# Kernel optimization log

Measured on AMD Instinct MI355X. Metric: run time of the kernel, lower is better.

## Reference

```python
import jax, jax.numpy as jnp
import numpy as np

B, C, C1, C2, H, W = 16, 64, 16, 64, 128, 128

def setup_inputs() -> dict:
    key = jax.random.key(0)
    ks = jax.random.split(key, 8)
    s1 = 1.0 / np.sqrt(C1)
    s2 = 1.0 / np.sqrt(C)
    return {
        "x": jax.random.normal(ks[0], (B, C, H, W), dtype=jnp.float32),
        "e": jax.random.normal(ks[1], (B, C1, H, W), dtype=jnp.float32),
        "W1": jax.random.uniform(ks[2], (C2, C1), jnp.float32, -s1, s1),
        "b1": jax.random.uniform(ks[3], (C2,), jnp.float32, -s1, s1),
        "W2": jax.random.uniform(ks[4], (C2, C), jnp.float32, -s2, s2),
        "b2": jax.random.uniform(ks[5], (C2,), jnp.float32, -s2, s2),
        "W3": jax.random.uniform(ks[6], (C2, C), jnp.float32, -s2, s2),
        "b3": jax.random.uniform(ks[7], (C2,), jnp.float32, -s2, s2),
    }

def _conv1x1(inp, Wm, bv):
    # (B,Cin,H,W) x (Cout,Cin) -> (B,Cout,H,W)
    return jnp.einsum('bchw,oc->bohw', inp, Wm) + bv[None, :, None, None]

def reference(x, e, W1, b1, W2, b2, W3, b3):
    Bn, _, Hn, Wn = x.shape
    Q = _conv1x1(e, W1, b1).reshape(-1, Hn, Wn)   # (B*C2, H, W)
    V = _conv1x1(x, W2, b2).reshape(-1, Hn, Wn)
    K = _conv1x1(x, W3, b3).reshape(-1, Hn, Wn)
    score = jnp.einsum('nhw,ngw->nhg', Q, V)      # (B*C2, H, H), no scaling
    attn = jax.nn.softmax(score, axis=-1)
    ctx = jnp.einsum('nhg,ngw->nhw', attn, K)     # (B*C2, H, W)
    return ctx.reshape(Bn, -1, Hn, Wn)
```

## Files before the change

kernel.cpp:

```cpp
#include <hip/hip_runtime.h>

typedef __bf16 bf16_t;
typedef __bf16 bf16x8 __attribute__((ext_vector_type(8)));
typedef float f32x4 __attribute__((ext_vector_type(4)));
typedef unsigned short u16x4_t __attribute__((ext_vector_type(4)));

#define HW 16384
#define LOG2E 1.44269504088896f

__device__ __forceinline__ bf16_t f2b(float f) {
  unsigned u = __builtin_bit_cast(unsigned, f);
  u += 0x7fff + ((u >> 16) & 1);
  unsigned short s = (unsigned short)(u >> 16);
  return __builtin_bit_cast(bf16_t, s);
}
__device__ __forceinline__ unsigned short b2u(bf16_t b) {
  return __builtin_bit_cast(unsigned short, b);
}
__device__ __forceinline__ int swz8(int row) { return ((row ^ (row >> 3)) & 7) << 4; }
__device__ __forceinline__ int swz4v(int row) { return (row ^ (row >> 2)) & 3; }

__global__ __launch_bounds__(256, 3) void qvk_kernel(
    const float* __restrict__ x, const float* __restrict__ e,
    const float* __restrict__ W1, const float* __restrict__ b1,
    const float* __restrict__ W2, const float* __restrict__ b2,
    const float* __restrict__ W3, const float* __restrict__ b3,
    bf16_t* __restrict__ Qg, bf16_t* __restrict__ Vg, bf16_t* __restrict__ Kg)
{
  __shared__ bf16_t lx[128 * 64];
  __shared__ bf16_t le[128 * 32];
  __shared__ bf16_t w2b[64 * 64];
  __shared__ bf16_t w3b[64 * 64];
  __shared__ bf16_t w1b[64 * 32];

  const int t = threadIdx.x;
  const int lane = t & 63;
  const int wv = t >> 6;
  const int b = blockIdx.x >> 7;
  const int p0 = (blockIdx.x & 127) << 7;
  const int lr = lane & 15;
  const int lg = lane >> 4;
  const int kq = lg << 3;

  const int li = lane & 31;
  const int h2 = lane >> 5;
  const int cbase = wv * 16 + h2 * 8;
  f32x4 xr[8];
#pragma unroll
  for (int j = 0; j < 8; ++j)
    xr[j] = *reinterpret_cast<const f32x4*>(
        x + (size_t)(b * 64 + cbase + j) * HW + p0 + li * 4);

  const int ec = t >> 4;
  const int ep = (t & 15) * 4;
  f32x4 er[2];
#pragma unroll
  for (int j = 0; j < 2; ++j)
    er[j] = *reinterpret_cast<const f32x4*>(
        e + (size_t)(b * 16 + ec) * HW + p0 + ep + j * 64);

  const int wo = t >> 2;
  const int wc = (t & 3) * 16;
  f32x4 w2r[4], w3r[4];
#pragma unroll
  for (int k = 0; k < 4; ++k) {
    w2r[k] = *reinterpret_cast<const f32x4*>(W2 + (size_t)wo * 64 + wc + k * 4);
    w3r[k] = *reinterpret_cast<const f32x4*>(W3 + (size_t)wo * 64 + wc + k * 4);
  }
  const int w1c = (t & 3) * 4;
  f32x4 w1r = *reinterpret_cast<const f32x4*>(W1 + (size_t)wo * 16 + w1c);

  float bv1[4], bv2[4], bv3[4];
#pragma unroll
  for (int nt = 0; nt < 4; ++nt) {
    bv1[nt] = b1[nt * 16 + lr];
    bv2[nt] = b2[nt * 16 + lr];
    bv3[nt] = b3[nt * 16 + lr];
  }

  {
    const int chunk = cbase >> 3;
#pragma unroll
    for (int r = 0; r < 4; ++r) {
      const int row = li * 4 + r;
      bf16x8 v;
#pragma unroll
      for (int j = 0; j < 8; ++j) v[j] = f2b(xr[j][r]);
      *reinterpret_cast<bf16x8*>(reinterpret_cast<char*>(lx)
          + row * 128 + ((chunk << 4) ^ swz8(row))) = v;
    }
  }
#pragma unroll
  for (int j = 0; j < 2; ++j)
#pragma unroll
    for (int r = 0; r < 4; ++r) {
      const int row = ep + j * 64 + r;
      const int byte = row * 64 + ((((ec >> 3) ^ swz4v(row)) << 4)) + (ec & 7) * 2;
      *reinterpret_cast<bf16_t*>(reinterpret_cast<char*>(le) + byte) = f2b(er[j][r]);
    }
  {
    const int row = t >> 1;
    const int chunk = 2 + (t & 1);
    bf16x8 zv;
#pragma unroll
    for (int k = 0; k < 8; ++k) zv[k] = f2b(0.0f);
    *reinterpret_cast<bf16x8*>(reinterpret_cast<char*>(le)
        + row * 64 + ((chunk ^ swz4v(row)) << 4)) = zv;
  }
  {
    const int ch0 = (t & 3) * 2;
    bf16x8 a, c2;
#pragma unroll
    for (int k = 0; k < 8; ++k) {
      a[k]  = f2b(w2r[k >> 2][k & 3]);
      c2[k] = f2b(w2r[2 + (k >> 2)][k & 3]);
    }
    *reinterpret_cast<bf16x8*>(reinterpret_cast<char*>(w2b)
        + wo * 128 + ((ch0 << 4) ^ swz8(wo))) = a;
    *reinterpret_cast<bf16x8*>(reinterpret_cast<char*>(w2b)
        + wo * 128 + (((ch0 + 1) << 4) ^ swz8(wo))) = c2;
#pragma unroll
    for (int k = 0; k < 8; ++k) {
      a[k]  = f2b(w3r[k >> 2][k & 3]);
      c2[k] = f2b(w3r[2 + (k >> 2)][k & 3]);
    }
    *reinterpret_cast<bf16x8*>(reinterpret_cast<char*>(w3b)
        + wo * 128 + ((ch0 << 4) ^ swz8(wo))) = a;
    *reinterpret_cast<bf16x8*>(reinterpret_cast<char*>(w3b)
        + wo * 128 + (((ch0 + 1) << 4) ^ swz8(wo))) = c2;
  }
  {
    typedef __bf16 bf16x4_ __attribute__((ext_vector_type(4)));
    bf16x4_ a;
#pragma unroll
    for (int k = 0; k < 4; ++k) a[k] = f2b(w1r[k]);
    const int byte = wo * 64 + (((w1c >> 3) ^ swz4v(wo)) << 4) + (w1c & 4) * 2;
    *reinterpret_cast<bf16x4_*>(reinterpret_cast<char*>(w1b) + byte) = a;
    if (t < 128) {
      const int row = t >> 1;
      const int chunk = 2 + (t & 1);
      bf16x8 zv;
#pragma unroll
      for (int k = 0; k < 8; ++k) zv[k] = f2b(0.0f);
      *reinterpret_cast<bf16x8*>(reinterpret_cast<char*>(w1b)
          + row * 64 + ((chunk ^ swz4v(row)) << 4)) = zv;
    }
  }
  __syncthreads();

  const int pw0 = wv << 5;

  auto ldx = [&](int row, int ce) -> bf16x8 {
    return *reinterpret_cast<const bf16x8*>(reinterpret_cast<const char*>(lx)
        + row * 128 + (((ce >> 3) << 4) ^ swz8(row)));
  };
  auto ldw = [&](const bf16_t* wb, int row, int ce) -> bf16x8 {
    return *reinterpret_cast<const bf16x8*>(reinterpret_cast<const char*>(wb)
        + row * 128 + (((ce >> 3) << 4) ^ swz8(row)));
  };
  auto ld64 = [&](const bf16_t* buf, int row, int ce) -> bf16x8 {
    return *reinterpret_cast<const bf16x8*>(reinterpret_cast<const char*>(buf)
        + row * 64 + (((ce >> 3) ^ swz4v(row)) << 4));
  };

  f32x4 acc[2][4];

  auto do_xtarget = [&](const bf16_t* wb, const float* bvv, bf16_t* __restrict__ G) {
#pragma unroll
    for (int mt = 0; mt < 2; ++mt)
#pragma unroll
      for (int nt = 0; nt < 4; ++nt) acc[mt][nt] = f32x4{0.f, 0.f, 0.f, 0.f};
#pragma unroll
    for (int kt = 0; kt < 2; ++kt) {
      bf16x8 Af[2], Bw[4];
#pragma unroll
      for (int mt = 0; mt < 2; ++mt) Af[mt] = ldx(pw0 + mt * 16 + lr, kt * 32 + kq);
#pragma unroll
      for (int nt = 0; nt < 4; ++nt) Bw[nt] = ldw(wb, nt * 16 + lr, kt * 32 + kq);
#pragma unroll
      for (int mt = 0; mt < 2; ++mt)
#pragma unroll
        for (int nt = 0; nt < 4; ++nt)
          acc[mt][nt] = __builtin_amdgcn_mfma_f32_16x16x32_bf16(Af[mt], Bw[nt], acc[mt][nt], 0, 0, 0);
    }
#pragma unroll
    for (int nt = 0; nt < 4; ++nt)
#pragma unroll
      for (int mt = 0; mt < 2; ++mt) {
        u16x4_t pk;
#pragma unroll
        for (int r = 0; r < 4; ++r) pk[r] = b2u(f2b(acc[mt][nt][r] + bvv[nt]));
        *reinterpret_cast<u16x4_t*>(G + (size_t)(b * 64 + nt * 16 + lr) * HW
                                      + p0 + pw0 + mt * 16 + (lg << 2)) = pk;
      }
  };

  do_xtarget(w2b, bv2, Vg);
  do_xtarget(w3b, bv3, Kg);

#pragma unroll
  for (int mt = 0; mt < 2; ++mt)
#pragma unroll
    for (int nt = 0; nt < 4; ++nt) acc[mt][nt] = f32x4{0.f, 0.f, 0.f, 0.f};
  {
    bf16x8 Af[2], Bw[4];
#pragma unroll
    for (int mt = 0; mt < 2; ++mt) Af[mt] = ld64(le, pw0 + mt * 16 + lr, kq);
#pragma unroll
    for (int nt = 0; nt < 4; ++nt) Bw[nt] = ld64(w1b, nt * 16 + lr, kq);
#pragma unroll
    for (int mt = 0; mt < 2; ++mt)
#pragma unroll
      for (int nt = 0; nt < 4; ++nt)
        acc[mt][nt] = __builtin_amdgcn_mfma_f32_16x16x32_bf16(Af[mt], Bw[nt], acc[mt][nt], 0, 0, 0);
  }
#pragma unroll
  for (int nt = 0; nt < 4; ++nt)
#pragma unroll
    for (int mt = 0; mt < 2; ++mt) {
      u16x4_t pk;
#pragma unroll
      for (int r = 0; r < 4; ++r) pk[r] = b2u(f2b(acc[mt][nt][r] + bv1[nt]));
      *reinterpret_cast<u16x4_t*>(Qg + (size_t)(b * 64 + nt * 16 + lr) * HW
                                    + p0 + pw0 + mt * 16 + (lg << 2)) = pk;
    }
}

__global__ __launch_bounds__(256, 2) void attn_kernel(
    const bf16_t* __restrict__ Qg, const bf16_t* __restrict__ Vg,
    const bf16_t* __restrict__ Kg, float* __restrict__ out)
{
  __shared__ bf16_t bufK[128 * 128];
  __shared__ bf16_t bufV[128 * 128];
  __shared__ float zl[128];

  const int n = blockIdx.x;
  const int t = threadIdx.x;
  const int lane = t & 63;
  const int wv = t >> 6;
  const int lr = lane & 15;
  const int lg = lane >> 4;
  const int kq = lg << 3;
  const int h0 = wv << 5;

  const bf16_t* Qn = Qg + (size_t)n * HW;
  const bf16_t* Vn = Vg + (size_t)n * HW;
  const bf16_t* Kn = Kg + (size_t)n * HW;

  bf16x8 vreg[8];
#pragma unroll
  for (int it = 0; it < 8; ++it)
    vreg[it] = *reinterpret_cast<const bf16x8*>(Vn + (it * 256 + t) * 8);

  const int wchunk = t & 15;
  const int grow = t >> 4;
  bf16x8 kreg[8];
#pragma unroll
  for (int it = 0; it < 8; ++it)
    kreg[it] = *reinterpret_cast<const bf16x8*>(Kn + (grow + 16 * it) * 128 + wchunk * 8);

  bf16x8 qf[4][2];
#pragma unroll
  for (int kt = 0; kt < 4; ++kt)
#pragma unroll
    for (int mt = 0; mt < 2; ++mt)
      qf[kt][mt] = *reinterpret_cast<const bf16x8*>(
          Qn + (h0 + mt * 16 + lr) * 128 + kt * 32 + kq);

#pragma unroll
  for (int it = 0; it < 8; ++it) {
    const int chunk = it * 256 + t;
    const int row = chunk >> 4;
    *reinterpret_cast<bf16x8*>(reinterpret_cast<char*>(bufV)
        + row * 256 + (((chunk & 15) << 4) ^ swz8(row))) = vreg[it];
  }
  __syncthreads();

  auto ldfrag = [&](const bf16_t* buf, int row, int c) -> bf16x8 {
    return *reinterpret_cast<const bf16x8*>(reinterpret_cast<const char*>(buf)
        + row * 256 + (((c << 1)) ^ swz8(row)));
  };

  f32x4 acc[2][8];
#pragma unroll
  for (int mt = 0; mt < 2; ++mt)
#pragma unroll
    for (int nt = 0; nt < 8; ++nt) acc[mt][nt] = f32x4{0.f, 0.f, 0.f, 0.f};
#pragma unroll
  for (int kt = 0; kt < 4; ++kt) {
#pragma unroll
    for (int nt = 0; nt < 8; ++nt) {
      bf16x8 Bv = ldfrag(bufV, nt * 16 + lr, kt * 32 + kq);
      acc[0][nt] = __builtin_amdgcn_mfma_f32_16x16x32_bf16(qf[kt][0], Bv, acc[0][nt], 0, 0, 0);
      acc[1][nt] = __builtin_amdgcn_mfma_f32_16x16x32_bf16(qf[kt][1], Bv, acc[1][nt], 0, 0, 0);
    }
  }

#pragma unroll
  for (int it = 0; it < 8; ++it) {
    const int g = grow + 16 * it;
#pragma unroll
    for (int j = 0; j < 8; ++j) {
      const int w = wchunk * 8 + j;
      *reinterpret_cast<bf16_t*>(reinterpret_cast<char*>(bufK)
          + w * 256 + ((g << 1) ^ swz8(w))) = kreg[it][j];
    }
  }

  float zrow[2][4];
#pragma unroll
  for (int mt = 0; mt < 2; ++mt) {
#pragma unroll
    for (int r = 0; r < 4; ++r) {
      float m = acc[mt][0][r];
#pragma unroll
      for (int nt = 1; nt < 8; ++nt) m = fmaxf(m, acc[mt][nt][r]);
      m = fmaxf(m, __shfl_xor(m, 1));
      m = fmaxf(m, __shfl_xor(m, 2));
      m = fmaxf(m, __shfl_xor(m, 4));
      m = fmaxf(m, __shfl_xor(m, 8));
      float z = 0.f;
#pragma unroll
      for (int nt = 0; nt < 8; ++nt) {
        float p = exp2f((acc[mt][nt][r] - m) * LOG2E);
        acc[mt][nt][r] = p;
        z += p;
      }
      z += __shfl_xor(z, 1);
      z += __shfl_xor(z, 2);
      z += __shfl_xor(z, 4);
      z += __shfl_xor(z, 8);
      zrow[mt][r] = z;
    }
  }
  __syncthreads();

#pragma unroll
  for (int mt = 0; mt < 2; ++mt) {
    const int rbase = h0 + mt * 16 + (lg << 2);
    if (lr == 0) {
#pragma unroll
      for (int r = 0; r < 4; ++r) zl[rbase + r] = 1.0f / zrow[mt][r];
    }
#pragma unroll
    for (int nt = 0; nt < 8; ++nt) {
#pragma unroll
      for (int r = 0; r < 4; ++r) {
        const int row = rbase + r;
        *reinterpret_cast<bf16_t*>(reinterpret_cast<char*>(bufV)
            + row * 256 + (((nt * 16 + lr) << 1) ^ swz8(row))) = f2b(acc[mt][nt][r]);
      }
    }
  }
  __syncthreads();

  f32x4 acc2[2][8];
#pragma unroll
  for (int mt = 0; mt < 2; ++mt)
#pragma unroll
    for (int nt = 0; nt < 8; ++nt) acc2[mt][nt] = f32x4{0.f, 0.f, 0.f, 0.f};
#pragma unroll
  for (int kt = 0; kt < 4; ++kt) {
    bf16x8 A0 = ldfrag(bufK, h0 + lr,      kt * 32 + kq);
    bf16x8 A1 = ldfrag(bufK, h0 + 16 + lr, kt * 32 + kq);
#pragma unroll
    for (int nt = 0; nt < 8; ++nt) {
      bf16x8 Bp = ldfrag(bufV, nt * 16 + lr, kt * 32 + kq);
      acc2[0][nt] = __builtin_amdgcn_mfma_f32_16x16x32_bf16(A0, Bp, acc2[0][nt], 0, 0, 0);
      acc2[1][nt] = __builtin_amdgcn_mfma_f32_16x16x32_bf16(A1, Bp, acc2[1][nt], 0, 0, 0);
    }
  }

  float* On = out + (size_t)n * HW;
#pragma unroll
  for (int nt = 0; nt < 8; ++nt) {
    const float zv = zl[nt * 16 + lr];
#pragma unroll
    for (int mt = 0; mt < 2; ++mt) {
      f32x4 o;
#pragma unroll
      for (int r = 0; r < 4; ++r) o[r] = acc2[mt][nt][r] * zv;
      *reinterpret_cast<f32x4*>(On + (size_t)(nt * 16 + lr) * 128
                                + h0 + mt * 16 + (lg << 2)) = o;
    }
  }
}

extern "C" void kernel_launch(void* const* d_in, const int* in_sizes, int n_in,
                              void* d_out, int out_size, void* d_ws, size_t ws_size,
                              hipStream_t stream) {
  const float* x  = (const float*)d_in[0];
  const float* e  = (const float*)d_in[1];
  const float* W1 = (const float*)d_in[2];
  const float* b1 = (const float*)d_in[3];
  const float* W2 = (const float*)d_in[4];
  const float* b2 = (const float*)d_in[5];
  const float* W3 = (const float*)d_in[6];
  const float* b3 = (const float*)d_in[7];
  float* out = (float*)d_out;

  bf16_t* Qg = (bf16_t*)d_ws;
  bf16_t* Vg = Qg + (size_t)1024 * HW;
  bf16_t* Kg = Vg + (size_t)1024 * HW;

  qvk_kernel<<<2048, 256, 0, stream>>>(x, e, W1, b1, W2, b2, W3, b3, Qg, Vg, Kg);
  attn_kernel<<<1024, 256, 0, stream>>>(Qg, Vg, Kg, out);
}
```

Before: 196.2 us.

## Stage projection outputs through LDS for coalesced stores; widen attention blocks to 8 waves

The projection kernel now writes each bf16 output tile into a swizzled shared buffer and then stores full contiguous 32-byte row segments to global memory, replacing the previous scattered 8-byte stores. The aim is better write coalescing for Q, V and K, at the cost of extra LDS traffic and two barriers per half-tile. Separately, the attention kernel moves from 4 to 8 waves per block, so each wave handles 16 rows instead of 32. This lowers per-thread register use and adds parallelism per block, but splits the same MFMA work across more waves with less fragment reuse.

```diff
diff --git a/kernel.cpp b/kernel.cpp
--- a/kernel.cpp
+++ b/kernel.cpp
@@ -32,6 +32,7 @@
   __shared__ bf16_t w2b[64 * 64];
   __shared__ bf16_t w3b[64 * 64];
   __shared__ bf16_t w1b[64 * 32];
+  __shared__ bf16_t rep[32 * 128];
 
   const int t = threadIdx.x;
   const int lane = t & 63;
@@ -165,6 +166,38 @@
 
   f32x4 acc[2][4];
 
+  auto store_repack = [&](const float* bvv, bf16_t* __restrict__ G) {
+#pragma unroll
+    for (int half = 0; half < 2; ++half) {
+#pragma unroll
+      for (int q = 0; q < 2; ++q) {
+        const int nt = half * 2 + q;
+        const int ro = q * 16 + lr;
+#pragma unroll
+        for (int mt = 0; mt < 2; ++mt) {
+          u16x4_t pk;
+#pragma unroll
+          for (int r = 0; r < 4; ++r) pk[r] = b2u(f2b(acc[mt][nt][r] + bvv[nt]));
+          const int byte = ro * 256 + ((((pw0 + mt * 16 + (lg << 2)) << 1)) ^ swz8(ro));
+          *reinterpret_cast<u16x4_t*>(reinterpret_cast<char*>(rep) + byte) = pk;
+        }
+      }
+      __syncthreads();
+      {
+        const int ro = t >> 3;
+        const int cb = (t & 7) * 32;
+        bf16x8 v0 = *reinterpret_cast<const bf16x8*>(
+            reinterpret_cast<const char*>(rep) + ro * 256 + (cb ^ swz8(ro)));
+        bf16x8 v1 = *reinterpret_cast<const bf16x8*>(
+            reinterpret_cast<const char*>(rep) + ro * 256 + ((cb + 16) ^ swz8(ro)));
+        bf16_t* gp = G + (size_t)(b * 64 + half * 32 + ro) * HW + p0 + (t & 7) * 16;
+        *reinterpret_cast<bf16x8*>(gp) = v0;
+        *reinterpret_cast<bf16x8*>(gp + 8) = v1;
+      }
+      __syncthreads();
+    }
+  };
+
   auto do_xtarget = [&](const bf16_t* wb, const float* bvv, bf16_t* __restrict__ G) {
 #pragma unroll
     for (int mt = 0; mt < 2; ++mt)
@@ -183,16 +216,7 @@
         for (int nt = 0; nt < 4; ++nt)
           acc[mt][nt] = __builtin_amdgcn_mfma_f32_16x16x32_bf16(Af[mt], Bw[nt], acc[mt][nt], 0, 0, 0);
     }
-#pragma unroll
-    for (int nt = 0; nt < 4; ++nt)
-#pragma unroll
-      for (int mt = 0; mt < 2; ++mt) {
-        u16x4_t pk;
-#pragma unroll
-        for (int r = 0; r < 4; ++r) pk[r] = b2u(f2b(acc[mt][nt][r] + bvv[nt]));
-        *reinterpret_cast<u16x4_t*>(G + (size_t)(b * 64 + nt * 16 + lr) * HW
-                                      + p0 + pw0 + mt * 16 + (lg << 2)) = pk;
-      }
+    store_repack(bvv, G);
   };
 
   do_xtarget(w2b, bv2, Vg);
@@ -214,19 +238,10 @@
       for (int nt = 0; nt < 4; ++nt)
         acc[mt][nt] = __builtin_amdgcn_mfma_f32_16x16x32_bf16(Af[mt], Bw[nt], acc[mt][nt], 0, 0, 0);
   }
-#pragma unroll
-  for (int nt = 0; nt < 4; ++nt)
-#pragma unroll
-    for (int mt = 0; mt < 2; ++mt) {
-      u16x4_t pk;
-#pragma unroll
-      for (int r = 0; r < 4; ++r) pk[r] = b2u(f2b(acc[mt][nt][r] + bv1[nt]));
-      *reinterpret_cast<u16x4_t*>(Qg + (size_t)(b * 64 + nt * 16 + lr) * HW
-                                    + p0 + pw0 + mt * 16 + (lg << 2)) = pk;
-    }
+  store_repack(bv1, Qg);
 }
 
-__global__ __launch_bounds__(256, 2) void attn_kernel(
+__global__ __launch_bounds__(512, 2) void attn_kernel(
     const bf16_t* __restrict__ Qg, const bf16_t* __restrict__ Vg,
     const bf16_t* __restrict__ Kg, float* __restrict__ out)
 {
@@ -241,35 +256,32 @@
   const int lr = lane & 15;
   const int lg = lane >> 4;
   const int kq = lg << 3;
-  const int h0 = wv << 5;
+  const int h0 = wv << 4;
 
   const bf16_t* Qn = Qg + (size_t)n * HW;
   const bf16_t* Vn = Vg + (size_t)n * HW;
   const bf16_t* Kn = Kg + (size_t)n * HW;
 
-  bf16x8 vreg[8];
-#pragma unroll
-  for (int it = 0; it < 8; ++it)
-    vreg[it] = *reinterpret_cast<const bf16x8*>(Vn + (it * 256 + t) * 8);
+  bf16x8 vreg[4];
+#pragma unroll
+  for (int it = 0; it < 4; ++it)
+    vreg[it] = *reinterpret_cast<const bf16x8*>(Vn + (it * 512 + t) * 8);
 
   const int wchunk = t & 15;
   const int grow = t >> 4;
-  bf16x8 kreg[8];
-#pragma unroll
-  for (int it = 0; it < 8; ++it)
-    kreg[it] = *reinterpret_cast<const bf16x8*>(Kn + (grow + 16 * it) * 128 + wchunk * 8);
-
-  bf16x8 qf[4][2];
+  bf16x8 kreg[4];
+#pragma unroll
+  for (int it = 0; it < 4; ++it)
+    kreg[it] = *reinterpret_cast<const bf16x8*>(Kn + (grow + 32 * it) * 128 + wchunk * 8);
+
+  bf16x8 qf[4];
 #pragma unroll
   for (int kt = 0; kt < 4; ++kt)
-#pragma unroll
-    for (int mt = 0; mt < 2; ++mt)
-      qf[kt][mt] = *reinterpret_cast<const bf16x8*>(
-          Qn + (h0 + mt * 16 + lr) * 128 + kt * 32 + kq);
-
-#pragma unroll
-  for (int it = 0; it < 8; ++it) {
-    const int chunk = it * 256 + t;
+    qf[kt] = *reinterpret_cast<const bf16x8*>(Qn + (h0 + lr) * 128 + kt * 32 + kq);
+
+#pragma unroll
+  for (int it = 0; it < 4; ++it) {
+    const int chunk = it * 512 + t;
     const int row = chunk >> 4;
     *reinterpret_cast<bf16x8*>(reinterpret_cast<char*>(bufV)
         + row * 256 + (((chunk & 15) << 4) ^ swz8(row))) = vreg[it];
@@ -281,24 +293,21 @@
         + row * 256 + (((c << 1)) ^ swz8(row)));
   };
 
-  f32x4 acc[2][8];
-#pragma unroll
-  for (int mt = 0; mt < 2; ++mt)
-#pragma unroll
-    for (int nt = 0; nt < 8; ++nt) acc[mt][nt] = f32x4{0.f, 0.f, 0.f, 0.f};
+  f32x4 acc[8];
+#pragma unroll
+  for (int nt = 0; nt < 8; ++nt) acc[nt] = f32x4{0.f, 0.f, 0.f, 0.f};
 #pragma unroll
   for (int kt = 0; kt < 4; ++kt) {
 #pragma unroll
     for (int nt = 0; nt < 8; ++nt) {
       bf16x8 Bv = ldfrag(bufV, nt * 16 + lr, kt * 32 + kq);
-      acc[0][nt] = __builtin_amdgcn_mfma_f32_16x16x32_bf16(qf[kt][0], Bv, acc[0][nt], 0, 0, 0);
-      acc[1][nt] = __builtin_amdgcn_mfma_f32_16x16x32_bf16(qf[kt][1], Bv, acc[1][nt], 0, 0, 0);
-    }
-  }
-
-#pragma unroll
-  for (int it = 0; it < 8; ++it) {
-    const int g = grow + 16 * it;
+      acc[nt] = __builtin_amdgcn_mfma_f32_16x16x32_bf16(qf[kt], Bv, acc[nt], 0, 0, 0);
+    }
+  }
+
+#pragma unroll
+  for (int it = 0; it < 4; ++it) {
+    const int g = grow + 32 * it;
 #pragma unroll
     for (int j = 0; j < 8; ++j) {
       const int w = wchunk * 8 + j;
@@ -307,40 +316,36 @@
     }
   }
 
-  float zrow[2][4];
-#pragma unroll
-  for (int mt = 0; mt < 2; ++mt) {
-#pragma unroll
-    for (int r = 0; r < 4; ++r) {
-      float m = acc[mt][0][r];
-#pragma unroll
-      for (int nt = 1; nt < 8; ++nt) m = fmaxf(m, acc[mt][nt][r]);
-      m = fmaxf(m, __shfl_xor(m, 1));
-      m = fmaxf(m, __shfl_xor(m, 2));
-      m = fmaxf(m, __shfl_xor(m, 4));
-      m = fmaxf(m, __shfl_xor(m, 8));
-      float z = 0.f;
-#pragma unroll
-      for (int nt = 0; nt < 8; ++nt) {
-        float p = exp2f((acc[mt][nt][r] - m) * LOG2E);
-        acc[mt][nt][r] = p;
-        z += p;
-      }
-      z += __shfl_xor(z, 1);
-      z += __shfl_xor(z, 2);
-      z += __shfl_xor(z, 4);
-      z += __shfl_xor(z, 8);
-      zrow[mt][r] = z;
-    }
+  float zrow[4];
+#pragma unroll
+  for (int r = 0; r < 4; ++r) {
+    float m = acc[0][r];
+#pragma unroll
+    for (int nt = 1; nt < 8; ++nt) m = fmaxf(m, acc[nt][r]);
+    m = fmaxf(m, __shfl_xor(m, 1));
+    m = fmaxf(m, __shfl_xor(m, 2));
+    m = fmaxf(m, __shfl_xor(m, 4));
+    m = fmaxf(m, __shfl_xor(m, 8));
+    float z = 0.f;
+#pragma unroll
+    for (int nt = 0; nt < 8; ++nt) {
+      float p = exp2f((acc[nt][r] - m) * LOG2E);
+      acc[nt][r] = p;
+      z += p;
+    }
+    z += __shfl_xor(z, 1);
+    z += __shfl_xor(z, 2);
+    z += __shfl_xor(z, 4);
+    z += __shfl_xor(z, 8);
+    zrow[r] = z;
   }
   __syncthreads();
 
-#pragma unroll
-  for (int mt = 0; mt < 2; ++mt) {
-    const int rbase = h0 + mt * 16 + (lg << 2);
+  {
+    const int rbase = h0 + (lg << 2);
     if (lr == 0) {
 #pragma unroll
-      for (int r = 0; r < 4; ++r) zl[rbase + r] = 1.0f / zrow[mt][r];
+      for (int r = 0; r < 4; ++r) zl[rbase + r] = 1.0f / zrow[r];
     }
 #pragma unroll
     for (int nt = 0; nt < 8; ++nt) {
@@ -348,26 +353,22 @@
       for (int r = 0; r < 4; ++r) {
         const int row = rbase + r;
         *reinterpret_cast<bf16_t*>(reinterpret_cast<char*>(bufV)
-            + row * 256 + (((nt * 16 + lr) << 1) ^ swz8(row))) = f2b(acc[mt][nt][r]);
+            + row * 256 + (((nt * 16 + lr) << 1) ^ swz8(row))) = f2b(acc[nt][r]);
       }
     }
   }
   __syncthreads();
 
-  f32x4 acc2[2][8];
-#pragma unroll
-  for (int mt = 0; mt < 2; ++mt)
-#pragma unroll
-    for (int nt = 0; nt < 8; ++nt) acc2[mt][nt] = f32x4{0.f, 0.f, 0.f, 0.f};
+  f32x4 acc2[8];
+#pragma unroll
+  for (int nt = 0; nt < 8; ++nt) acc2[nt] = f32x4{0.f, 0.f, 0.f, 0.f};
 #pragma unroll
   for (int kt = 0; kt < 4; ++kt) {
-    bf16x8 A0 = ldfrag(bufK, h0 + lr,      kt * 32 + kq);
-    bf16x8 A1 = ldfrag(bufK, h0 + 16 + lr, kt * 32 + kq);
+    bf16x8 A0 = ldfrag(bufK, h0 + lr, kt * 32 + kq);
 #pragma unroll
     for (int nt = 0; nt < 8; ++nt) {
       bf16x8 Bp = ldfrag(bufV, nt * 16 + lr, kt * 32 + kq);
-      acc2[0][nt] = __builtin_amdgcn_mfma_f32_16x16x32_bf16(A0, Bp, acc2[0][nt], 0, 0, 0);
-      acc2[1][nt] = __builtin_amdgcn_mfma_f32_16x16x32_bf16(A1, Bp, acc2[1][nt], 0, 0, 0);
+      acc2[nt] = __builtin_amdgcn_mfma_f32_16x16x32_bf16(A0, Bp, acc2[nt], 0, 0, 0);
     }
   }
 
@@ -375,14 +376,11 @@
 #pragma unroll
   for (int nt = 0; nt < 8; ++nt) {
     const float zv = zl[nt * 16 + lr];
-#pragma unroll
-    for (int mt = 0; mt < 2; ++mt) {
-      f32x4 o;
-#pragma unroll
-      for (int r = 0; r < 4; ++r) o[r] = acc2[mt][nt][r] * zv;
-      *reinterpret_cast<f32x4*>(On + (size_t)(nt * 16 + lr) * 128
-                                + h0 + mt * 16 + (lg << 2)) = o;
-    }
+    f32x4 o;
+#pragma unroll
+    for (int r = 0; r < 4; ++r) o[r] = acc2[nt][r] * zv;
+    *reinterpret_cast<f32x4*>(On + (size_t)(nt * 16 + lr) * 128
+                              + h0 + (lg << 2)) = o;
   }
 }
 
@@ -404,5 +402,5 @@
   bf16_t* Kg = Vg + (size_t)1024 * HW;
 
   qvk_kernel<<<2048, 256, 0, stream>>>(x, e, W1, b1, W2, b2, W3, b3, Qg, Vg, Kg);
-  attn_kernel<<<1024, 256, 0, stream>>>(Qg, Vg, Kg, out);
+  attn_kernel<<<1024, 512, 0, stream>>>(Qg, Vg, Kg, out);
 }
```

Measured after the change: 203.2 us. 3.6% more time.
